# Kernel tuning notes

Measured on AMD Instinct MI355X. Metric: run time of the kernel, lower is better.

The kernel has to match this reference:

```python
import jax, jax.numpy as jnp
import numpy as np

ALPHA = 0.25
GAMMA = 2.0
EPS = 1e-8
COST_CLASS = 1.0
COST_BBOX = 1.0
COST_GIOU = 1.0


def segment_cw_to_t1t2(x):
    # x: [..., 2] = (center, width) -> (t1, t2)
    c, w = x[..., 0], x[..., 1]
    return jnp.stack([c - 0.5 * w, c + 0.5 * w], axis=-1)


def segment_iou(a, b):
    # a: [N, 2], b: [M, 2] -> pairwise IoU [N, M]
    lt = jnp.maximum(a[:, None, 0], b[None, :, 0])
    rb = jnp.minimum(a[:, None, 1], b[None, :, 1])
    inter = jnp.clip(rb - lt, 0.0)
    union = (a[:, 1] - a[:, 0])[:, None] + (b[:, 1] - b[:, 0])[None, :] - inter
    return inter / jnp.maximum(union, EPS)


def setup_inputs() -> dict:
    key = jax.random.key(0)
    k1, k2, k3, k4, k5, k6 = jax.random.split(key, 6)
    bs, Q, n_cls, M = 16, 2000, 80, 1024
    pred_logits = jax.random.normal(k1, (bs, Q, n_cls), dtype=jnp.float32)
    # boxes layout: [t1, t2, center, width] with t1<=t2 and width>0 (valid segments)
    p_t = jnp.sort(jax.random.uniform(k2, (bs, Q, 2), dtype=jnp.float32), axis=-1)
    p_cw = jax.random.uniform(k3, (bs, Q, 2), dtype=jnp.float32) * jnp.array([1.0, 0.5]) + jnp.array([0.0, 0.05])
    pred_boxes = jnp.concatenate([p_t, p_cw], axis=-1)
    t_t = jnp.sort(jax.random.uniform(k4, (M, 2), dtype=jnp.float32), axis=-1)
    t_cw = jax.random.uniform(k5, (M, 2), dtype=jnp.float32) * jnp.array([1.0, 0.5]) + jnp.array([0.0, 0.05])
    tgt_bbox = jnp.concatenate([t_t, t_cw], axis=-1)
    tgt_ids = jax.random.randint(k6, (M,), 0, n_cls, dtype=jnp.int64 if jax.config.jax_enable_x64 else jnp.int32)
    return {"pred_logits": pred_logits, "pred_boxes": pred_boxes,
            "tgt_ids": tgt_ids, "tgt_bbox": tgt_bbox}


def reference(pred_logits, pred_boxes, tgt_ids, tgt_bbox):
    bs, Q, _ = pred_logits.shape
    out_prob = jax.nn.softmax(pred_logits.reshape(bs * Q, -1), axis=-1)  # [bs*Q, n_cls]
    out_bbox = pred_boxes.reshape(bs * Q, 4)
    # focal-style classification cost
    neg_cost = (1.0 - ALPHA) * out_prob ** GAMMA * (-jnp.log1p(-out_prob + EPS))
    pos_cost = ALPHA * (1.0 - out_prob) ** GAMMA * (-jnp.log(out_prob + EPS))
    cost_class = pos_cost[:, tgt_ids] - neg_cost[:, tgt_ids]  # [bs*Q, M]
    # L1 box cost (cdist p=1)
    cost_bbox = jnp.sum(jnp.abs(out_bbox[:, None, :] - tgt_bbox[None, :, :]), axis=-1)
    # GIoU-style cost: average of IoU over (c,w)->t1t2 segments and raw t1t2 segments
    cost_giou = -(segment_iou(segment_cw_to_t1t2(out_bbox[:, 2:]), segment_cw_to_t1t2(tgt_bbox[:, 2:]))
                  + segment_iou(out_bbox[:, :2], tgt_bbox[:, :2])) / 2.0
    C = COST_BBOX * cost_bbox + COST_CLASS * cost_class + COST_GIOU * cost_giou
    return C.reshape(bs, Q, -1)
```

## Files before the change

kernel.cpp:

```cpp
#include <hip/hip_runtime.h>
#include <math.h>

#define ALPHA 0.25f
#define EPS 1e-8f

typedef float f4v __attribute__((ext_vector_type(4)));

constexpr int NCLS = 80;
constexpr int Mn = 1024;
constexpr int RPB = 8;

__global__ __launch_bounds__(256, 5) void matcher_kernel(
    const float* __restrict__ logits,
    const float* __restrict__ pboxes,
    const int*   __restrict__ tids,
    const float* __restrict__ tboxes,
    float* __restrict__ out)
{
    __shared__ float cls[RPB][NCLS];

    const int tid  = threadIdx.x;
    const int row0 = blockIdx.x * RPB;

    const int j0 = tid * 4;
    float t1[4], t2[4], tc[4], th[4], wr[4];
    int id[4];
    #pragma unroll
    for (int k = 0; k < 4; ++k) {
        float4 b = *(const float4*)(tboxes + (size_t)(j0 + k) * 4);
        t1[k] = b.x;
        t2[k] = b.y;
        tc[k] = b.z;
        th[k] = 0.5f * b.w;
        wr[k] = b.y - b.x;
        id[k] = tids[j0 + k];
    }

    if (tid < 160) {
        ((float4*)&cls[0][0])[tid] =
            ((const float4*)(logits + (size_t)row0 * NCLS))[tid];
    }
    __syncthreads();

    {
        const int r = tid >> 5;
        const int c = tid & 31;
        const int c2 = (c < 16) ? c + 64 : c;
        float l0 = cls[r][c];
        float l1 = cls[r][c + 32];
        float l2 = cls[r][c2];
        float e0 = __expf(l0);
        float e1 = __expf(l1);
        float e2 = (c < 16) ? __expf(l2) : 0.0f;
        float s = e0 + e1 + e2;
        #pragma unroll
        for (int off = 16; off; off >>= 1) s += __shfl_xor(s, off);
        float inv_s = __builtin_amdgcn_rcpf(s);
        float p0 = e0 * inv_s, p1 = e1 * inv_s, p2 = e2 * inv_s;
        float o0 = 1.0f - p0, o1 = 1.0f - p1, o2 = 1.0f - p2;
        float cc0 = ALPHA * o0 * o0 * (-__logf(p0 + EPS))
                  - (1.0f - ALPHA) * p0 * p0 * (-__logf(o0 + EPS));
        float cc1 = ALPHA * o1 * o1 * (-__logf(p1 + EPS))
                  - (1.0f - ALPHA) * p1 * p1 * (-__logf(o1 + EPS));
        float cc2 = ALPHA * o2 * o2 * (-__logf(p2 + EPS))
                  - (1.0f - ALPHA) * p2 * p2 * (-__logf(o2 + EPS));
        cls[r][c]      = cc0;
        cls[r][c + 32] = cc1;
        if (c < 16) cls[r][c + 64] = cc2;
    }
    __syncthreads();

    #pragma unroll 2
    for (int r = 0; r < RPB; ++r) {
        const float4 pb = *(const float4*)(pboxes + (size_t)(row0 + r) * 4);
        const float pwr = pb.y - pb.x;
        const float phw = 0.5f * pb.w;

        f4v res;
        #pragma unroll
        for (int k = 0; k < 4; ++k) {
            float d1 = pb.x - t1[k];
            float d2 = pb.y - t2[k];
            float dc = pb.z - tc[k];
            float dw = phw - th[k];
            float ab = fabsf(d1) + fabsf(d2);
            float db = ab + fmaf(fabsf(dw), 2.0f, fabsf(dc));
            float P1 = fmaf(2.0f, th[k], pb.w);
            float A1 = fmaxf(P1 - (fabsf(dc - dw) + fabsf(dc + dw)), 0.0f);
            float D1 = fmaxf(fmaf(2.0f, P1, -A1), 2.0f * EPS);
            float P2 = pwr + wr[k];
            float A2 = fmaxf(P2 - ab, 0.0f);
            float D2 = fmaxf(fmaf(2.0f, P2, -A2), 2.0f * EPS);
            float num = A1 * D2 + A2 * D1;
            float inv = __builtin_amdgcn_rcpf(D1 * D2);
            res[k] = fmaf(num * inv, -0.5f, db + cls[r][id[k]]);
        }
        __builtin_nontemporal_store(res,
            (f4v*)(out + (size_t)(row0 + r) * Mn + j0));
    }
}

extern "C" void kernel_launch(void* const* d_in, const int* in_sizes, int n_in,
                              void* d_out, int out_size, void* d_ws, size_t ws_size,
                              hipStream_t stream) {
    const float* logits = (const float*)d_in[0];
    const float* pboxes = (const float*)d_in[1];
    const int*   tids   = (const int*)d_in[2];
    const float* tboxes = (const float*)d_in[3];
    float* out = (float*)d_out;

    const int total_rows = in_sizes[0] / NCLS;
    const int nblocks = total_rows / RPB;
    matcher_kernel<<<nblocks, 256, 0, stream>>>(logits, pboxes, tids, tboxes, out);
}
```

Before: 35.84 us.

## Make each wave own eight rows independently and drop block-wide barriers

Work is restructured so each 64-lane wave handles eight query rows on its own. The wave computes its softmax and focal class cost with 8-lane shuffles into a per-wave shared buffer, then loops over four 256-target groups. Block-level __syncthreads is replaced by a wave barrier, and prediction boxes are held as wave-uniform values via readfirstlane so they can sit in scalar registers. The aim is to remove block synchronization stalls and raise compute per block, at the cost of reloading target boxes per group and having four times fewer blocks.

```diff
diff --git a/kernel.cpp b/kernel.cpp
--- a/kernel.cpp
+++ b/kernel.cpp
@@ -8,7 +8,13 @@
 
 constexpr int NCLS = 80;
 constexpr int Mn = 1024;
-constexpr int RPB = 8;
+constexpr int RPW = 8;
+constexpr int WPB = 4;
+constexpr int RPB = RPW * WPB;
+
+__device__ __forceinline__ float rfl(float x) {
+    return __int_as_float(__builtin_amdgcn_readfirstlane(__float_as_int(x)));
+}
 
 __global__ __launch_bounds__(256, 5) void matcher_kernel(
     const float* __restrict__ logits,
@@ -17,86 +23,89 @@
     const float* __restrict__ tboxes,
     float* __restrict__ out)
 {
-    __shared__ float cls[RPB][NCLS];
+    __shared__ float cc[WPB][RPW][NCLS];
 
     const int tid  = threadIdx.x;
-    const int row0 = blockIdx.x * RPB;
+    const int wid  = tid >> 6;
+    const int lane = tid & 63;
+    const int row0 = __builtin_amdgcn_readfirstlane(blockIdx.x * RPB + wid * RPW);
 
-    const int j0 = tid * 4;
-    float t1[4], t2[4], tc[4], th[4], wr[4];
-    int id[4];
+    {
+        const int r   = lane >> 3;
+        const int sub = lane & 7;
+        const float* lrow = logits + (size_t)(row0 + r) * NCLS + sub;
+        float e[10], s = 0.0f;
+        #pragma unroll
+        for (int k = 0; k < 10; ++k) {
+            e[k] = __expf(lrow[8 * k]);
+            s += e[k];
+        }
+        s += __shfl_xor(s, 1);
+        s += __shfl_xor(s, 2);
+        s += __shfl_xor(s, 4);
+        float inv_s = __builtin_amdgcn_rcpf(s);
+        float* ccrow = &cc[wid][r][sub];
+        #pragma unroll
+        for (int k = 0; k < 10; ++k) {
+            float p = e[k] * inv_s;
+            float o = 1.0f - p;
+            float v = ALPHA * o * o * (-__logf(p + EPS))
+                    - (1.0f - ALPHA) * p * p * (-__logf(o + EPS));
+            ccrow[8 * k] = v;
+        }
+    }
+    __builtin_amdgcn_wave_barrier();
+
+    float rp0[RPW], rp1[RPW], rpc[RPW], rpw[RPW], rhw[RPW], rwr[RPW];
     #pragma unroll
-    for (int k = 0; k < 4; ++k) {
-        float4 b = *(const float4*)(tboxes + (size_t)(j0 + k) * 4);
-        t1[k] = b.x;
-        t2[k] = b.y;
-        tc[k] = b.z;
-        th[k] = 0.5f * b.w;
-        wr[k] = b.y - b.x;
-        id[k] = tids[j0 + k];
+    for (int r = 0; r < RPW; ++r) {
+        float4 pb = *(const float4*)(pboxes + (size_t)(row0 + r) * 4);
+        rp0[r] = rfl(pb.x);
+        rp1[r] = rfl(pb.y);
+        rpc[r] = rfl(pb.z);
+        rpw[r] = rfl(pb.w);
+        rhw[r] = rfl(0.5f * pb.w);
+        rwr[r] = rfl(pb.y - pb.x);
     }
 
-    if (tid < 160) {
-        ((float4*)&cls[0][0])[tid] =
-            ((const float4*)(logits + (size_t)row0 * NCLS))[tid];
-    }
-    __syncthreads();
-
-    {
-        const int r = tid >> 5;
-        const int c = tid & 31;
-        const int c2 = (c < 16) ? c + 64 : c;
-        float l0 = cls[r][c];
-        float l1 = cls[r][c + 32];
-        float l2 = cls[r][c2];
-        float e0 = __expf(l0);
-        float e1 = __expf(l1);
-        float e2 = (c < 16) ? __expf(l2) : 0.0f;
-        float s = e0 + e1 + e2;
-        #pragma unroll
-        for (int off = 16; off; off >>= 1) s += __shfl_xor(s, off);
-        float inv_s = __builtin_amdgcn_rcpf(s);
-        float p0 = e0 * inv_s, p1 = e1 * inv_s, p2 = e2 * inv_s;
-        float o0 = 1.0f - p0, o1 = 1.0f - p1, o2 = 1.0f - p2;
-        float cc0 = ALPHA * o0 * o0 * (-__logf(p0 + EPS))
-                  - (1.0f - ALPHA) * p0 * p0 * (-__logf(o0 + EPS));
-        float cc1 = ALPHA * o1 * o1 * (-__logf(p1 + EPS))
-                  - (1.0f - ALPHA) * p1 * p1 * (-__logf(o1 + EPS));
-        float cc2 = ALPHA * o2 * o2 * (-__logf(p2 + EPS))
-                  - (1.0f - ALPHA) * p2 * p2 * (-__logf(o2 + EPS));
-        cls[r][c]      = cc0;
-        cls[r][c + 32] = cc1;
-        if (c < 16) cls[r][c + 64] = cc2;
-    }
-    __syncthreads();
-
-    #pragma unroll 2
-    for (int r = 0; r < RPB; ++r) {
-        const float4 pb = *(const float4*)(pboxes + (size_t)(row0 + r) * 4);
-        const float pwr = pb.y - pb.x;
-        const float phw = 0.5f * pb.w;
-
-        f4v res;
+    #pragma unroll 1
+    for (int tg = 0; tg < 4; ++tg) {
+        const int j0 = tg * 256 + lane * 4;
+        int4 idv = *(const int4*)(tids + j0);
+        const int id[4] = {idv.x, idv.y, idv.z, idv.w};
+        float t1[4], t2[4], tc_[4], th[4], wr[4];
         #pragma unroll
         for (int k = 0; k < 4; ++k) {
-            float d1 = pb.x - t1[k];
-            float d2 = pb.y - t2[k];
-            float dc = pb.z - tc[k];
-            float dw = phw - th[k];
-            float ab = fabsf(d1) + fabsf(d2);
-            float db = ab + fmaf(fabsf(dw), 2.0f, fabsf(dc));
-            float P1 = fmaf(2.0f, th[k], pb.w);
-            float A1 = fmaxf(P1 - (fabsf(dc - dw) + fabsf(dc + dw)), 0.0f);
-            float D1 = fmaxf(fmaf(2.0f, P1, -A1), 2.0f * EPS);
-            float P2 = pwr + wr[k];
-            float A2 = fmaxf(P2 - ab, 0.0f);
-            float D2 = fmaxf(fmaf(2.0f, P2, -A2), 2.0f * EPS);
-            float num = A1 * D2 + A2 * D1;
-            float inv = __builtin_amdgcn_rcpf(D1 * D2);
-            res[k] = fmaf(num * inv, -0.5f, db + cls[r][id[k]]);
+            float4 b = *(const float4*)(tboxes + (size_t)(j0 + k) * 4);
+            t1[k] = b.x; t2[k] = b.y; tc_[k] = b.z;
+            th[k] = 0.5f * b.w;
+            wr[k] = b.y - b.x;
         }
-        __builtin_nontemporal_store(res,
-            (f4v*)(out + (size_t)(row0 + r) * Mn + j0));
+        #pragma unroll
+        for (int r = 0; r < RPW; ++r) {
+            const float* ccr = &cc[wid][r][0];
+            f4v res;
+            #pragma unroll
+            for (int k = 0; k < 4; ++k) {
+                float d1 = rp0[r] - t1[k];
+                float d2 = rp1[r] - t2[k];
+                float dc = rpc[r] - tc_[k];
+                float dw = rhw[r] - th[k];
+                float ab = fabsf(d1) + fabsf(d2);
+                float db = ab + fmaf(fabsf(dw), 2.0f, fabsf(dc));
+                float P1 = fmaf(2.0f, th[k], rpw[r]);
+                float A1 = fmaxf(P1 - (fabsf(dc - dw) + fabsf(dc + dw)), 0.0f);
+                float D1 = fmaxf(fmaf(2.0f, P1, -A1), 2.0f * EPS);
+                float P2 = rwr[r] + wr[k];
+                float A2 = fmaxf(P2 - ab, 0.0f);
+                float D2 = fmaxf(fmaf(2.0f, P2, -A2), 2.0f * EPS);
+                float num = A1 * D2 + A2 * D1;
+                float inv = __builtin_amdgcn_rcpf(D1 * D2);
+                res[k] = fmaf(num * inv, -0.5f, db + ccr[id[k]]);
+            }
+            __builtin_nontemporal_store(res,
+                (f4v*)(out + (size_t)(row0 + r) * Mn + j0));
+        }
     }
 }
 
```

Measured after the change: 38.67 us. 7.9% more time.
